# Kernel tuning notes

Measured on AMD Instinct MI355X. Metric: run time of the kernel, lower is better.

Reference implementation:

```python
import jax, jax.numpy as jnp
import numpy as np

B, L = 64, 200
NQ = 1024          # n_question == output_dim
NPID = 4096
D = 256            # q_embed_dim
H = 512            # hidden_dim
Q = 1024           # output_dim
L2 = 1e-05


def setup_inputs() -> dict:
    key = jax.random.key(0)
    ks = jax.random.split(key, 20)
    q_data = jax.random.randint(ks[0], (B, L), 1, NQ + 1)          # question ids in [1, NQ]
    ans = jax.random.randint(ks[1], (B, L), 0, 2)
    qa_data = q_data + NQ * ans                                     # encoded (q, answer)
    pid_data = jax.random.randint(ks[2], (B, L), 0, NPID + 1)
    matrix = jax.random.uniform(ks[3], (Q, Q), jnp.float32) * 0.05  # p_c_relations
    u = jax.random.uniform(ks[4], (B, L))
    target = jnp.where(u < 0.1, -1.0, jnp.where(u < 0.55, 0.0, 1.0)).astype(jnp.float32)
    s = 0.05
    q_emb = jax.random.normal(ks[5], (NQ + 1, D), jnp.float32) * s
    qa_emb = jax.random.normal(ks[6], (2, D), jnp.float32) * s
    q_emb_diff = jax.random.normal(ks[7], (NQ + 1, D), jnp.float32) * s
    qa_emb_diff = jax.random.normal(ks[8], (2 * NQ + 1, D), jnp.float32) * s
    diff_parm = jax.random.normal(ks[9], (NPID + 1, 1), jnp.float32) * s
    gs = 1.0 / np.sqrt(H).astype(np.float32)
    w_ih = jax.random.uniform(ks[10], (3 * H, 2 * D), jnp.float32, -gs, gs)
    w_hh = jax.random.uniform(ks[11], (3 * H, H), jnp.float32, -gs, gs)
    b_ih = jax.random.uniform(ks[12], (3 * H,), jnp.float32, -gs, gs)
    b_hh = jax.random.uniform(ks[13], (3 * H,), jnp.float32, -gs, gs)
    fc_w = jax.random.normal(ks[14], (Q, H), jnp.float32) * 0.02
    fc_b = jnp.zeros((Q,), jnp.float32)
    return dict(q_data=q_data, qa_data=qa_data, pid_data=pid_data, matrix=matrix,
                target=target, q_emb=q_emb, qa_emb=qa_emb, q_emb_diff=q_emb_diff,
                qa_emb_diff=qa_emb_diff, diff_parm=diff_parm, w_ih=w_ih, w_hh=w_hh,
                b_ih=b_ih, b_hh=b_hh, fc_w=fc_w, fc_b=fc_b)


def _gru(x, w_ih, w_hh, b_ih, b_hh):
    # PyTorch GRU, single layer, batch_first. x: [B, L, In]
    xg = jnp.einsum('bli,gi->blg', x, w_ih) + b_ih          # [B, L, 3H]
    def step(h, xg_t):
        hg = h @ w_hh.T + b_hh
        xr, xz, xn = jnp.split(xg_t, 3, axis=-1)
        hr, hz, hn = jnp.split(hg, 3, axis=-1)
        r = jax.nn.sigmoid(xr + hr)
        z = jax.nn.sigmoid(xz + hz)
        n = jnp.tanh(xn + r * hn)
        h_new = (1.0 - z) * n + z * h
        return h_new, h_new
    h0 = jnp.zeros((x.shape[0], w_hh.shape[1]), x.dtype)
    _, hs = jax.lax.scan(step, h0, xg.transpose(1, 0, 2))
    return hs.transpose(1, 0, 2)                             # [B, L, H]


def reference(q_data, qa_data, pid_data, matrix, target, q_emb, qa_emb,
              q_emb_diff, qa_emb_diff, diff_parm, w_ih, w_hh, b_ih, b_hh,
              fc_w, fc_b):
    q_embed = q_emb[q_data]                                  # [B, L, D]
    qa = (qa_data - q_data) // NQ                            # answer in {0,1}
    qa_embed = qa_emb[qa] + q_embed
    pid_embed = diff_parm[pid_data]                          # [B, L, 1]
    q_embed2 = q_embed + pid_embed * q_emb_diff[q_data]
    qa_embed2 = qa_embed + pid_embed * qa_emb_diff[qa]
    c_reg = (pid_embed ** 2).sum() * L2

    x = jnp.concatenate([qa_embed2, q_embed2], axis=-1)      # [B, L, 2D]
    gru_out = _gru(x, w_ih, w_hh, b_ih, b_hh)
    gru_out = jnp.einsum('blh,qh->blq', gru_out, fc_w) + fc_b  # [B, L, Q]

    got = jnp.einsum('blq,kq->blk', gru_out, matrix)         # [B, L, Q]
    master = jnp.where(got >= 0.4, 1.0, got)                 # threshold-to-1 only
    # mastery of the question asked at step t: master[b, t, q-1]
    mvals = jnp.take_along_axis(master, (q_data - 1)[..., None], axis=2)[..., 0]  # [B, L]

    f32 = jnp.float32
    eq = (q_data[:, :, None] == q_data[:, None, :]).astype(f32)   # [B, t, k]
    t_idx = jnp.arange(L)
    tri_strict = (t_idx[:, None] > t_idx[None, :]).astype(f32)    # k < t
    tri_incl = (t_idx[:, None] >= t_idx[None, :]).astype(f32)     # k <= t
    mast = (mvals == 1.0).astype(f32)
    notm = (mvals == 0.0).astype(f32)
    qa1 = (qa == 1).astype(f32)
    qa0 = 1.0 - qa1
    base = eq * tri_strict                                        # [B, L, L]
    mc = jnp.einsum('btk,bk->bt', base, qa1 * mast)   # master_correct
    mi = jnp.einsum('btk,bk->bt', base, qa0 * mast)   # master_incorrect
    nmc = jnp.einsum('btk,bk->bt', base, qa0 * notm)  # no_master_correct
    aa = jnp.einsum('btk,tk->bt', eq, tri_incl)       # answered_all (>= 1)

    arB = jnp.arange(B)
    idx = q_data - 1

    def dina_step(carry, xs):
        guess, slip = carry                            # [B, Q] each
        i_t, m_t, qa_t, mc_t, mi_t, nmc_t, aa_t = xs   # [B] each
        g_upd = jnp.where(m_t == 1.0, mc_t / aa_t,
                          jnp.where(qa_t == 0, 1.0 - nmc_t / aa_t, nmc_t / aa_t))
        upd_slip = (m_t == 1.0) & (qa_t == 0)
        new_g = jnp.where(upd_slip, guess[arB, i_t], g_upd)
        new_s = jnp.where(upd_slip, mi_t / aa_t, slip[arB, i_t])
        guess = guess.at[arB, i_t].set(new_g)
        slip = slip.at[arB, i_t].set(new_s)
        p = (1.0 - new_s) * (m_t * new_g + (1.0 - new_s) * (1.0 - m_t))
        return (guess, slip), p

    init = (jnp.zeros((B, Q), f32), jnp.zeros((B, Q), f32))
    xs = (idx.T, mvals.T, qa.T, mc.T, mi.T, nmc.T, aa.T)
    _, ps = jax.lax.scan(dina_step, init, xs)          # [L, B]
    preds = ps.T.reshape(-1)                           # [B*L]

    labels = target.reshape(-1)
    mask = labels > -0.9
    preds_d = jax.lax.stop_gradient(preds)             # torch detaches via torch.tensor()
    mse_sum = (((preds_d - labels) ** 2) * mask.astype(f32)).sum()
    loss = mse_sum + c_reg
    return (loss, jax.nn.sigmoid(preds_d), mask.sum())
```

## Files before the change

### kernel.cpp

```cpp
#include <hip/hip_runtime.h>
#include <hip/hip_bf16.h>
#include <math.h>

#define BB 64
#define LL 200
#define NQ 1024
#define DD 256
#define HH 512
#define QQ 1024
#define G3 1536
#define BL 12800
#define GBLK 256
#define NWRK 130

#define OFF_ACC   ((size_t)0)
#define OFF_CELLS ((size_t)16)
#define OFF_HA    ((size_t)1056)
#define OFF_AQ    (OFF_HA + 65536)
#define OFF_DQ    (OFF_AQ + 1574400)
#define OFF_BQA   (OFF_DQ + 1574400)
#define OFF_CQA   (OFF_BQA + 3072)
#define OFF_WSUM  (OFF_CQA + 3072)
#define OFF_FCWT  (OFF_WSUM + 393216)
#define OFF_M2    (OFF_FCWT + 524288)
#define OFF_MB    (OFF_M2 + 524288)
#define OFF_XG    (OFF_MB + 1024)
#define OFF_GRUT  (OFF_XG + 19660800)
#define OFF_QINT  (OFF_GRUT + 6553600)
#define OFF_QAINT (OFF_QINT + 12800)
#define OFF_PIDF  (OFF_QAINT + 12800)
#define OFF_MVAL  (OFF_PIDF + 12800)
#define OFF_MC    (OFF_MVAL + 12800)
#define OFF_MI    (OFF_MC + 12800)
#define OFF_NMC   (OFF_MI + 12800)
#define OFF_AA    (OFF_NMC + 12800)
#define OFF_PREDS (OFF_AA + 12800)

typedef float f32x4 __attribute__((ext_vector_type(4)));

__device__ __forceinline__ float wave_sum64(float v) {
    #pragma unroll
    for (int o = 32; o > 0; o >>= 1) v += __shfl_down(v, o, 64);
    return v;
}

__device__ __forceinline__ f32x4 llc_load4(const float* p) {
    f32x4 v;
    asm volatile("global_load_dwordx4 %0, %1, off sc0 sc1" : "=v"(v) : "v"(p));
    return v;
}
__device__ __forceinline__ void llc_wait2(f32x4& a, f32x4& b) {
    asm volatile("s_waitcnt vmcnt(0)" : "+v"(a), "+v"(b));
}
__device__ __forceinline__ void llc_store1(float* p, float v) {
    asm volatile("global_store_dword %0, %1, off sc0 sc1" :: "v"(p), "v"(v) : "memory");
}

__device__ __forceinline__ float quad_sum(float v) {
    float t1 = __int_as_float(__builtin_amdgcn_update_dpp(
        0, __float_as_int(v), 0xB1, 0xF, 0xF, true));
    v += t1;
    float t2 = __int_as_float(__builtin_amdgcn_update_dpp(
        0, __float_as_int(v), 0x4E, 0xF, 0xF, true));
    return v + t2;
}

__global__ __launch_bounds__(256) void prep_meta(
    const int* __restrict__ q_data, const int* __restrict__ qa_data,
    const int* __restrict__ pid_data, const float* __restrict__ diff_parm,
    int* __restrict__ qint, int* __restrict__ qaint, float* __restrict__ pidf,
    float* __restrict__ acc)
{
    int r = blockIdx.x * 256 + threadIdx.x;
    float pp = 0.f;
    if (r < BL) {
        int q = q_data[r];
        qint[r] = q;
        qaint[r] = (qa_data[r] - q) / NQ;
        float pid = diff_parm[pid_data[r]];
        pidf[r] = pid;
        pp = pid * pid;
    }
    pp = wave_sum64(pp);
    __shared__ float sm[4];
    int lane = threadIdx.x & 63, w = threadIdx.x >> 6;
    if (lane == 0) sm[w] = pp;
    __syncthreads();
    if (threadIdx.x == 0) atomicAdd(&acc[0], sm[0] + sm[1] + sm[2] + sm[3]);
}

__global__ __launch_bounds__(256) void wsum_kernel(const float* __restrict__ w_ih,
                                                   float* __restrict__ wsum)
{
    int g = blockIdx.x, d = threadIdx.x;
    wsum[(size_t)g * DD + d] = w_ih[(size_t)g * 2 * DD + d] + w_ih[(size_t)g * 2 * DD + DD + d];
}

__global__ __launch_bounds__(256) void gemm_nt_dual(
    const float* __restrict__ A0, const float* __restrict__ A1, int lda,
    const float* __restrict__ B0, const float* __restrict__ B1, int ldb0, int ldb1,
    float* __restrict__ C0, float* __restrict__ C1, int ldc,
    int M, int N, int K,
    const float* __restrict__ bias0, const float* __restrict__ bias1)
{
    const int z = blockIdx.z;
    const float* A = z ? A1 : A0;
    const float* B = z ? B1 : B0;
    float* C = z ? C1 : C0;
    const int ldb = z ? ldb1 : ldb0;
    const float* bias = z ? bias1 : bias0;

    __shared__ float As[16][65];
    __shared__ float Bs[16][65];
    const int bm = blockIdx.y * 64, bn = blockIdx.x * 64;
    const int tid = threadIdx.x;
    const int tx = tid & 15, ty = tid >> 4;
    const int mm = tid >> 4, kk = tid & 15;
    float acc[4][4] = {};
    float ar[4], br[4];
    #pragma unroll
    for (int i = 0; i < 4; ++i) {
        int m = bm + mm + 16 * i;
        ar[i] = (m < M) ? A[(size_t)m * lda + kk] : 0.f;
        int n = bn + mm + 16 * i;
        br[i] = (n < N) ? B[(size_t)n * ldb + kk] : 0.f;
    }
    for (int k0 = 0; k0 < K; k0 += 16) {
        #pragma unroll
        for (int i = 0; i < 4; ++i) { As[kk][mm + 16 * i] = ar[i]; Bs[kk][mm + 16 * i] = br[i]; }
        __syncthreads();
        int kn = k0 + 16;
        if (kn < K) {
            #pragma unroll
            for (int i = 0; i < 4; ++i) {
                int m = bm + mm + 16 * i;
                ar[i] = (m < M) ? A[(size_t)m * lda + kn + kk] : 0.f;
                int n = bn + mm + 16 * i;
                br[i] = (n < N) ? B[(size_t)n * ldb + kn + kk] : 0.f;
            }
        }
        #pragma unroll
        for (int kq = 0; kq < 16; ++kq) {
            float a[4], b[4];
            #pragma unroll
            for (int i = 0; i < 4; ++i) a[i] = As[kq][ty * 4 + i];
            #pragma unroll
            for (int j = 0; j < 4; ++j) b[j] = Bs[kq][tx * 4 + j];
            #pragma unroll
            for (int i = 0; i < 4; ++i)
                #pragma unroll
                for (int j = 0; j < 4; ++j) acc[i][j] += a[i] * b[j];
        }
        __syncthreads();
    }
    #pragma unroll
    for (int i = 0; i < 4; ++i) {
        int m = bm + ty * 4 + i;
        if (m >= M) continue;
        #pragma unroll
        for (int j = 0; j < 4; ++j) {
            int n = bn + tx * 4 + j;
            if (n >= N) continue;
            C[(size_t)m * ldc + n] = acc[i][j] + (bias ? bias[n] : 0.f);
        }
    }
}

__global__ __launch_bounds__(512) void xgt_kernel(
    const float* __restrict__ Aq, const float* __restrict__ Bqa,
    const float* __restrict__ Cqa, const float* __restrict__ Dq,
    const int* __restrict__ qint, const int* __restrict__ qaint,
    const float* __restrict__ pidf, float* __restrict__ xgT)
{
    const int t = blockIdx.x;
    __shared__ float tile[64][129];
    __shared__ int qs[BB];
    __shared__ int qas[BB];
    __shared__ float ps[BB];
    const int tid = threadIdx.x;
    if (tid < BB) {
        qs[tid] = qint[tid * LL + t];
        qas[tid] = qaint[tid * LL + t];
        ps[tid] = pidf[tid * LL + t];
    }
    __syncthreads();
    for (int g0 = 0; g0 < G3; g0 += 128) {
        #pragma unroll
        for (int it = 0; it < 16; ++it) {
            int idx = it * 512 + tid;
            int b = idx >> 7, gg = idx & 127;
            int g = g0 + gg;
            int q = qs[b], qa = qas[b];
            float pid = ps[b];
            tile[b][gg] = Aq[(size_t)q * G3 + g] + Bqa[(size_t)qa * G3 + g]
                        + pid * (Cqa[(size_t)qa * G3 + g] + Dq[(size_t)q * G3 + g]);
        }
        __syncthreads();
        #pragma unroll
        for (int it = 0; it < 16; ++it) {
            int idx = it * 512 + tid;
            int gg = idx >> 6, b = idx & 63;
            xgT[((size_t)t * G3 + g0 + gg) * BB + b] = tile[b][gg];
        }
        __syncthreads();
    }
}

__global__ __launch_bounds__(512) void gru_persist(
    const float* __restrict__ xgT,
    const float* __restrict__ w_hh,
    const float* __restrict__ b_hh,
    float* __restrict__ hA,
    float* __restrict__ gruT2,
    unsigned int* __restrict__ cells,
    const float* __restrict__ matrix,
    const float* __restrict__ fc_w,
    const float* __restrict__ fc_b,
    float* __restrict__ M2,
    float* __restrict__ mb)
{
    __shared__ float hs[8][512];
    __shared__ float part[8][3][16][8];
    __shared__ float As[16][65];
    __shared__ float Bs[16][65];

    const int tid = threadIdx.x;
    const int bid = blockIdx.x;

    if (bid >= GBLK) {
        const int widx = bid - GBLK;
        if (widx >= 128) {
            const int wv2 = tid >> 6, lane2 = tid & 63;
            const int kb = (widx - 128) * 512 + wv2 * 64;
            for (int i = 0; i < 64; ++i) {
                const float* mrow = matrix + (size_t)(kb + i) * QQ;
                float sacc = 0.f;
                #pragma unroll
                for (int j = 0; j < 16; ++j)
                    sacc += mrow[lane2 + 64 * j] * fc_b[lane2 + 64 * j];
                sacc = wave_sum64(sacc);
                if (lane2 == 0) mb[kb + i] = sacc;
            }
            return;
        }
        const int bm = (widx >> 3) * 64, bn = (widx & 7) * 64;
        const int mm = tid >> 4, kk = tid & 15;
        const int nn = tid & 31, k2 = tid >> 5;
        const int tx = tid & 15, ty = tid >> 4;
        float acc[2][4] = {};
        for (int k0 = 0; k0 < QQ; k0 += 16) {
            if (k0) __syncthreads();
            As[kk][mm]      = matrix[(size_t)(bm + mm) * QQ + k0 + kk];
            As[kk][mm + 32] = matrix[(size_t)(bm + mm + 32) * QQ + k0 + kk];
            Bs[k2][nn]      = fc_w[(size_t)(k0 + k2) * HH + bn + nn];
            Bs[k2][nn + 32] = fc_w[(size_t)(k0 + k2) * HH + bn + nn + 32];
            __syncthreads();
            #pragma unroll
            for (int kq = 0; kq < 16; ++kq) {
                float a0 = As[kq][ty * 2], a1 = As[kq][ty * 2 + 1];
                #pragma unroll
                for (int j = 0; j < 4; ++j) {
                    float bv = Bs[kq][tx * 4 + j];
                    acc[0][j] += a0 * bv;
                    acc[1][j] += a1 * bv;
                }
            }
        }
        #pragma unroll
        for (int i = 0; i < 2; ++i)
            #pragma unroll
            for (int j = 0; j < 4; ++j)
                M2[(size_t)(bm + ty * 2 + i) * HH + bn + tx * 4 + j] = acc[i][j];
        return;
    }

    __builtin_amdgcn_s_setprio(1);

    const int bg = bid >> 5;
    const int j0 = (bid & 31) * 16;
    const int wv = tid >> 6;
    const int lane = tid & 63;
    const int g = lane >> 2;
    const int s = lane & 3;

    f32x4 ws4[3][4];
    #pragma unroll
    for (int gate = 0; gate < 3; ++gate)
        #pragma unroll
        for (int q = 0; q < 4; ++q)
            ws4[gate][q] = *(const f32x4*)&w_hh[
                (size_t)(gate * HH + j0 + g) * HH + wv * 64 + q * 16 + s * 4];

    const int eu = tid >> 3;
    const int eb = tid & 7;
    float bhr = 0.f, bhz = 0.f, bhn = 0.f;
    if (tid < 128) {
        bhr = b_hh[j0 + eu];
        bhz = b_hh[HH + j0 + eu];
        bhn = b_hh[2 * HH + j0 + eu];
    }

    const int b0 = lane >> 4;
    const int c0 = (lane & 15) * 4;

    for (int t = 0; t < LL; ++t) {
        float xr = 0.f, xz = 0.f, xn = 0.f;
        if (tid < 128) {
            const float* xb = xgT + (size_t)t * G3 * BB;
            int col = bg * 8 + eb;
            xr = xb[(size_t)(j0 + eu) * BB + col];
            xz = xb[(size_t)(HH + j0 + eu) * BB + col];
            xn = xb[(size_t)(2 * HH + j0 + eu) * BB + col];
        }
        if (t && tid < 64) {
            const unsigned want = (unsigned)t;
            for (;;) {
                unsigned v = want;
                if (lane < 32)
                    v = __hip_atomic_load(&cells[(bg * 32 + lane) * 4],
                                          __ATOMIC_RELAXED, __HIP_MEMORY_SCOPE_AGENT);
                if (__all((int)(v >= want))) break;
                __builtin_amdgcn_s_sleep(2);
            }
        }
        __syncthreads();

        {
            const float* hcur = hA + (size_t)(t & 1) * (HH * BB);
            const float* p0 = hcur + (size_t)(bg * 8 + b0) * HH + wv * 64 + c0;
            f32x4 va = llc_load4(p0);
            f32x4 vb = llc_load4(p0 + 4 * HH);
            llc_wait2(va, vb);
            *(f32x4*)&hs[wv][b0 * 64 + ((c0 + 8 * b0) & 63)] = va;
            *(f32x4*)&hs[wv][(b0 + 4) * 64 + ((c0 + 8 * b0 + 32) & 63)] = vb;
        }

        float acc[3][8];
        #pragma unroll
        for (int gate = 0; gate < 3; ++gate) {
            #pragma unroll
            for (int b = 0; b < 8; ++b) acc[gate][b] = 0.f;
        }
        #pragma unroll
        for (int q = 0; q < 4; ++q) {
            const int cb = q * 16 + s * 4;
            #pragma unroll
            for (int b = 0; b < 8; ++b) {
                f32x4 h4 = *(const f32x4*)&hs[wv][b * 64 + ((cb + 8 * b) & 63)];
                #pragma unroll
                for (int gate = 0; gate < 3; ++gate) {
                    acc[gate][b] += ws4[gate][q].x * h4.x + ws4[gate][q].y * h4.y
                                  + ws4[gate][q].z * h4.z + ws4[gate][q].w * h4.w;
                }
            }
        }

        #pragma unroll
        for (int gate = 0; gate < 3; ++gate)
            #pragma unroll
            for (int b = 0; b < 8; ++b)
                acc[gate][b] = quad_sum(acc[gate][b]);

        if (s < 3) {
            const int rot = (2 * ((g >> 2) + s)) & 7;
            #pragma unroll
            for (int hp = 0; hp < 4; ++hp) {
                const int b = hp * 2;
                float e0 = (s == 0) ? acc[0][b]     : (s == 1) ? acc[1][b]     : acc[2][b];
                float e1 = (s == 0) ? acc[0][b + 1] : (s == 1) ? acc[1][b + 1] : acc[2][b + 1];
                const int bp = (b + rot) & 7;
                *(float2*)&part[wv][s][g][bp] = make_float2(e0, e1);
            }
        }
        __syncthreads();

        if (tid < 128) {
            const int rb = eu >> 2;
            const int bp0 = (eb + 2 * (rb + 0)) & 7;
            const int bp1 = (eb + 2 * (rb + 1)) & 7;
            const int bp2 = (eb + 2 * (rb + 2)) & 7;
            float sg0 = 0.f, sg1 = 0.f, sg2 = 0.f;
            #pragma unroll
            for (int w = 0; w < 8; ++w) {
                sg0 += part[w][0][eu][bp0];
                sg1 += part[w][1][eu][bp1];
                sg2 += part[w][2][eu][bp2];
            }
            const int ku = j0 + eu;
            float hprev = hs[ku >> 6][eb * 64 + (((ku & 63) + 8 * eb) & 63)];
            float rg = 1.f / (1.f + expf(-(xr + sg0 + bhr)));
            float zg = 1.f / (1.f + expf(-(xz + sg1 + bhz)));
            float ng = tanhf(xn + rg * (sg2 + bhn));
            float hn = (1.f - zg) * ng + zg * hprev;
            llc_store1(hA + (size_t)((t + 1) & 1) * (HH * BB)
                          + (size_t)(bg * 8 + eb) * HH + ku, hn);
            gruT2[((size_t)t * BB + bg * 8 + eb) * HH + ku] = hn;
            asm volatile("s_waitcnt vmcnt(0)" ::: "memory");
        }
        __syncthreads();
        if (tid == 0 && t + 1 < LL)
            __hip_atomic_store(&cells[bid * 4], (unsigned)(t + 1),
                               __ATOMIC_RELAXED, __HIP_MEMORY_SCOPE_AGENT);
    }
}

__global__ __launch_bounds__(256) void mval_kernel(
    const float* __restrict__ gruT2,
    const float* __restrict__ M2,
    const float* __restrict__ mb,
    const int* __restrict__ qint,
    float* __restrict__ mval)
{
    int t = blockIdx.x;
    int wave = threadIdx.x >> 6, l = threadIdx.x & 63;
    for (int ii = 0; ii < 16; ++ii) {
        int b = wave * 16 + ii;
        int q = qint[b * LL + t] - 1;
        const float4* hp = (const float4*)(gruT2 + ((size_t)t * BB + b) * HH);
        const float4* mp = (const float4*)(M2 + (size_t)q * HH);
        float4 h0 = hp[l], m0 = mp[l];
        float4 h1 = hp[64 + l], m1 = mp[64 + l];
        float acc = h0.x * m0.x + h0.y * m0.y + h0.z * m0.z + h0.w * m0.w
                  + h1.x * m1.x + h1.y * m1.y + h1.z * m1.z + h1.w * m1.w;
        acc = wave_sum64(acc);
        if (l == 0) {
            float sv = acc + mb[q];
            mval[b * LL + t] = (sv >= 0.4f) ? 1.0f : sv;
        }
    }
}

__global__ __launch_bounds__(256) void stats_kernel(
    const int* __restrict__ qint, const int* __restrict__ qaint,
    const float* __restrict__ mval,
    float* __restrict__ mc, float* __restrict__ mi,
    float* __restrict__ nmc, float* __restrict__ aa)
{
    int b = blockIdx.x, tid = threadIdx.x;
    __shared__ int qs[LL];
    __shared__ int qas[LL];
    __shared__ float mv[LL];
    if (tid < LL) {
        qs[tid] = qint[b * LL + tid];
        qas[tid] = qaint[b * LL + tid];
        mv[tid] = mval[b * LL + tid];
    }
    __syncthreads();
    int t = tid;
    if (t < LL) {
        int qt = qs[t];
        float smc = 0.f, smi = 0.f, snmc = 0.f, saa = 0.f;
        for (int k = 0; k <= t; ++k) {
            if (qs[k] == qt) {
                saa += 1.f;
                if (k < t) {
                    float mk = (mv[k] == 1.f) ? 1.f : 0.f;
                    float nk = (mv[k] == 0.f) ? 1.f : 0.f;
                    float a1 = (qas[k] == 1) ? 1.f : 0.f;
                    smc += a1 * mk;
                    smi += (1.f - a1) * mk;
                    snmc += (1.f - a1) * nk;
                }
            }
        }
        mc[b * LL + t] = smc;
        mi[b * LL + t] = smi;
        nmc[b * LL + t] = snmc;
        aa[b * LL + t] = saa;
    }
}

__global__ __launch_bounds__(256) void dina_kernel(
    const int* __restrict__ qint, const int* __restrict__ qaint,
    const float* __restrict__ mval,
    const float* __restrict__ mc, const float* __restrict__ mi,
    const float* __restrict__ nmc, const float* __restrict__ aa,
    float* __restrict__ preds)
{
    int b = blockIdx.x, tid = threadIdx.x;
    __shared__ float guess[QQ], slip[QQ];
    __shared__ float s_m[LL], s_mc[LL], s_mi[LL], s_nmc[LL], s_aa[LL];
    __shared__ int s_i[LL], s_qa[LL];
    for (int i = tid; i < QQ; i += 256) { guess[i] = 0.f; slip[i] = 0.f; }
    if (tid < LL) {
        s_m[tid] = mval[b * LL + tid];
        s_mc[tid] = mc[b * LL + tid];
        s_mi[tid] = mi[b * LL + tid];
        s_nmc[tid] = nmc[b * LL + tid];
        s_aa[tid] = aa[b * LL + tid];
        s_i[tid] = qint[b * LL + tid] - 1;
        s_qa[tid] = qaint[b * LL + tid];
    }
    __syncthreads();
    if (tid == 0) {
        for (int t = 0; t < LL; ++t) {
            int i = s_i[t];
            float m = s_m[t];
            int qa = s_qa[t];
            float aat = s_aa[t];
            float g_upd = (m == 1.f) ? s_mc[t] / aat
                          : ((qa == 0) ? 1.f - s_nmc[t] / aat : s_nmc[t] / aat);
            bool us = (m == 1.f) && (qa == 0);
            float ng = us ? guess[i] : g_upd;
            float ns = us ? s_mi[t] / aat : slip[i];
            guess[i] = ng;
            slip[i] = ns;
            preds[b * LL + t] = (1.f - ns) * (m * ng + (1.f - ns) * (1.f - m));
        }
    }
}

__global__ __launch_bounds__(256) void loss_kernel(
    const float* __restrict__ preds, const float* __restrict__ target,
    float* __restrict__ out, float* __restrict__ acc)
{
    int r = blockIdx.x * 256 + threadIdx.x;
    float lm = 0.f, lc = 0.f;
    if (r < BL) {
        float p = preds[r], lab = target[r];
        float msk = (lab > -0.9f) ? 1.f : 0.f;
        float d = p - lab;
        lm = d * d * msk;
        lc = msk;
        out[1 + r] = 1.f / (1.f + expf(-p));
    }
    lm = wave_sum64(lm);
    lc = wave_sum64(lc);
    __shared__ float sm[4], sc[4];
    int lane = threadIdx.x & 63, w = threadIdx.x >> 6;
    if (lane == 0) { sm[w] = lm; sc[w] = lc; }
    __syncthreads();
    if (threadIdx.x == 0) {
        atomicAdd(&acc[1], sm[0] + sm[1] + sm[2] + sm[3]);
        atomicAdd(&acc[2], sc[0] + sc[1] + sc[2] + sc[3]);
    }
}

__global__ void final_kernel(const float* __restrict__ acc, float* __restrict__ out)
{
    out[0] = acc[1] + acc[0] * 1e-5f;
    out[1 + BL] = acc[2];
}

extern "C" void kernel_launch(void* const* d_in, const int* in_sizes, int n_in,
                              void* d_out, int out_size, void* d_ws, size_t ws_size,
                              hipStream_t stream) {
    const int* q_data = (const int*)d_in[0];
    const int* qa_data = (const int*)d_in[1];
    const int* pid_data = (const int*)d_in[2];
    const float* matrix = (const float*)d_in[3];
    const float* target = (const float*)d_in[4];
    const float* q_emb = (const float*)d_in[5];
    const float* qa_emb = (const float*)d_in[6];
    const float* q_emb_diff = (const float*)d_in[7];
    const float* qa_emb_diff = (const float*)d_in[8];
    const float* diff_parm = (const float*)d_in[9];
    const float* w_ih = (const float*)d_in[10];
    const float* w_hh = (const float*)d_in[11];
    const float* b_ih = (const float*)d_in[12];
    const float* b_hh = (const float*)d_in[13];
    const float* fc_w = (const float*)d_in[14];
    const float* fc_b = (const float*)d_in[15];
    float* out = (float*)d_out;
    float* W = (float*)d_ws;

    float* acc = W + OFF_ACC;
    unsigned int* cells = (unsigned int*)(W + OFF_CELLS);
    float* hA = W + OFF_HA;
    float* Aq = W + OFF_AQ;
    float* Dq = W + OFF_DQ;
    float* Bqa = W + OFF_BQA;
    float* Cqa = W + OFF_CQA;
    float* wsum = W + OFF_WSUM;
    float* M2 = W + OFF_M2;
    float* mb = W + OFF_MB;
    float* xgT = W + OFF_XG;
    float* gruT2 = W + OFF_GRUT;
    int* qint = (int*)(W + OFF_QINT);
    int* qaint = (int*)(W + OFF_QAINT);
    float* pidf = W + OFF_PIDF;
    float* mval = W + OFF_MVAL;
    float* mc = W + OFF_MC;
    float* mi = W + OFF_MI;
    float* nmc = W + OFF_NMC;
    float* aa = W + OFF_AA;
    float* preds = W + OFF_PREDS;

    hipMemsetAsync(W, 0, (OFF_HA + 2 * HH * BB) * sizeof(float), stream);

    prep_meta<<<50, 256, 0, stream>>>(q_data, qa_data, pid_data, diff_parm,
                                      qint, qaint, pidf, acc);
    wsum_kernel<<<G3, 256, 0, stream>>>(w_ih, wsum);

    gemm_nt_dual<<<dim3(24, 1, 2), 256, 0, stream>>>(
        qa_emb, qa_emb_diff, DD, w_ih, w_ih, 2 * DD, 2 * DD,
        Bqa, Cqa, G3, 2, G3, DD, b_ih, nullptr);
    gemm_nt_dual<<<dim3(24, 17, 2), 256, 0, stream>>>(
        q_emb, q_emb_diff, DD, wsum, w_ih + DD, DD, 2 * DD,
        Aq, Dq, G3, NQ + 1, G3, DD, nullptr, nullptr);

    xgt_kernel<<<LL, 512, 0, stream>>>(Aq, Bqa, Cqa, Dq, qint, qaint, pidf, xgT);

    gru_persist<<<GBLK + NWRK, 512, 0, stream>>>(xgT, w_hh, b_hh, hA, gruT2, cells,
                                                 matrix, fc_w, fc_b, M2, mb);

    mval_kernel<<<LL, 256, 0, stream>>>(gruT2, M2, mb, qint, mval);
    stats_kernel<<<BB, 256, 0, stream>>>(qint, qaint, mval, mc, mi, nmc, aa);
    dina_kernel<<<BB, 256, 0, stream>>>(qint, qaint, mval, mc, mi, nmc, aa, preds);
    loss_kernel<<<50, 256, 0, stream>>>(preds, target, out, acc);
    final_kernel<<<1, 1, 0, stream>>>(acc, out);
}
```

Before: 1.184 ms.

## Interleave M2/mb side GEMM into idle GRU waves across timesteps

Removes the extra worker blocks that computed M2 = matrix·fc_w and mb = matrix·fc_b alongside the persistent GRU. That work is now spread across the recurrent loop: waves 2-7 of each GRU block compute an 8x64 M2 tile, one k-slice of 8 per timestep for the first 128 steps, and the remaining slots do mb rows at staggered steps. The aim is to use idle wave time during the serial recurrence and drop the extra blocks and the setprio hack. The risk is that the added global loads per step lengthen the GRU critical path, since the wave barrier sync now waits on those waves.

New measurement: 1.405 ms. 18.6% more time.

```diff
diff --git a/kernel.cpp b/kernel.cpp
--- a/kernel.cpp
+++ b/kernel.cpp
@@ -11,7 +11,6 @@
 #define G3 1536
 #define BL 12800
 #define GBLK 256
-#define NWRK 130
 
 #define OFF_ACC   ((size_t)0)
 #define OFF_CELLS ((size_t)16)
@@ -221,61 +220,9 @@
 {
     __shared__ float hs[8][512];
     __shared__ float part[8][3][16][8];
-    __shared__ float As[16][65];
-    __shared__ float Bs[16][65];
 
     const int tid = threadIdx.x;
     const int bid = blockIdx.x;
-
-    if (bid >= GBLK) {
-        const int widx = bid - GBLK;
-        if (widx >= 128) {
-            const int wv2 = tid >> 6, lane2 = tid & 63;
-            const int kb = (widx - 128) * 512 + wv2 * 64;
-            for (int i = 0; i < 64; ++i) {
-                const float* mrow = matrix + (size_t)(kb + i) * QQ;
-                float sacc = 0.f;
-                #pragma unroll
-                for (int j = 0; j < 16; ++j)
-                    sacc += mrow[lane2 + 64 * j] * fc_b[lane2 + 64 * j];
-                sacc = wave_sum64(sacc);
-                if (lane2 == 0) mb[kb + i] = sacc;
-            }
-            return;
-        }
-        const int bm = (widx >> 3) * 64, bn = (widx & 7) * 64;
-        const int mm = tid >> 4, kk = tid & 15;
-        const int nn = tid & 31, k2 = tid >> 5;
-        const int tx = tid & 15, ty = tid >> 4;
-        float acc[2][4] = {};
-        for (int k0 = 0; k0 < QQ; k0 += 16) {
-            if (k0) __syncthreads();
-            As[kk][mm]      = matrix[(size_t)(bm + mm) * QQ + k0 + kk];
-            As[kk][mm + 32] = matrix[(size_t)(bm + mm + 32) * QQ + k0 + kk];
-            Bs[k2][nn]      = fc_w[(size_t)(k0 + k2) * HH + bn + nn];
-            Bs[k2][nn + 32] = fc_w[(size_t)(k0 + k2) * HH + bn + nn + 32];
-            __syncthreads();
-            #pragma unroll
-            for (int kq = 0; kq < 16; ++kq) {
-                float a0 = As[kq][ty * 2], a1 = As[kq][ty * 2 + 1];
-                #pragma unroll
-                for (int j = 0; j < 4; ++j) {
-                    float bv = Bs[kq][tx * 4 + j];
-                    acc[0][j] += a0 * bv;
-                    acc[1][j] += a1 * bv;
-                }
-            }
-        }
-        #pragma unroll
-        for (int i = 0; i < 2; ++i)
-            #pragma unroll
-            for (int j = 0; j < 4; ++j)
-                M2[(size_t)(bm + ty * 2 + i) * HH + bn + tx * 4 + j] = acc[i][j];
-        return;
-    }
-
-    __builtin_amdgcn_s_setprio(1);
-
     const int bg = bid >> 5;
     const int j0 = (bid & 31) * 16;
     const int wv = tid >> 6;
@@ -303,7 +250,49 @@
     const int b0 = lane >> 4;
     const int c0 = (lane & 15) * 4;
 
+    const int slot = bid * 6 + (wv - 2);
+    const bool do_m2 = (wv >= 2) && (slot < 1024);
+    const int r0 = (slot >> 3) << 3;
+    const int n0 = (slot & 7) << 6;
+    const bool do_mb = (wv >= 2) && (slot >= 1024);
+    const int mbrow = (slot - 1024) * 2;
+    const int mbstep = 64 + ((slot - 1024) & 63);
+    float m2acc[8] = {};
+
     for (int t = 0; t < LL; ++t) {
+        if (do_m2) {
+            if (t < 128) {
+                const int k0 = t * 8;
+                float bcol[8];
+                #pragma unroll
+                for (int j = 0; j < 8; ++j)
+                    bcol[j] = fc_w[(size_t)(k0 + j) * HH + n0 + lane];
+                #pragma unroll
+                for (int i = 0; i < 8; ++i) {
+                    f32x4 a0 = *(const f32x4*)&matrix[(size_t)(r0 + i) * QQ + k0];
+                    f32x4 a1 = *(const f32x4*)&matrix[(size_t)(r0 + i) * QQ + k0 + 4];
+                    m2acc[i] += a0.x * bcol[0] + a0.y * bcol[1] + a0.z * bcol[2]
+                              + a0.w * bcol[3] + a1.x * bcol[4] + a1.y * bcol[5]
+                              + a1.z * bcol[6] + a1.w * bcol[7];
+                }
+            } else if (t == 128) {
+                #pragma unroll
+                for (int i = 0; i < 8; ++i)
+                    M2[(size_t)(r0 + i) * HH + n0 + lane] = m2acc[i];
+            }
+        } else if (do_mb && t == mbstep) {
+            #pragma unroll
+            for (int rr = 0; rr < 2; ++rr) {
+                const float* mrow = matrix + (size_t)(mbrow + rr) * QQ;
+                float sacc = 0.f;
+                #pragma unroll
+                for (int j = 0; j < 16; ++j)
+                    sacc += mrow[lane + 64 * j] * fc_b[lane + 64 * j];
+                sacc = wave_sum64(sacc);
+                if (lane == 0) mb[mbrow + rr] = sacc;
+            }
+        }
+
         float xr = 0.f, xz = 0.f, xn = 0.f;
         if (tid < 128) {
             const float* xb = xgT + (size_t)t * G3 * BB;
@@ -601,8 +590,8 @@
 
     xgt_kernel<<<LL, 512, 0, stream>>>(Aq, Bqa, Cqa, Dq, qint, qaint, pidf, xgT);
 
-    gru_persist<<<GBLK + NWRK, 512, 0, stream>>>(xgT, w_hh, b_hh, hA, gruT2, cells,
-                                                 matrix, fc_w, fc_b, M2, mb);
+    gru_persist<<<GBLK, 512, 0, stream>>>(xgT, w_hh, b_hh, hA, gruT2, cells,
+                                          matrix, fc_w, fc_b, M2, mb);
 
     mval_kernel<<<LL, 256, 0, stream>>>(gruT2, M2, mb, qint, mval);
     stats_kernel<<<BB, 256, 0, stream>>>(qint, qaint, mval, mc, mi, nmc, aa);
```

## Fuse input-gate gather into GRU loop and split M2 GEMM out

Applied to the files above, without the earlier changes.

Removes the xgt_kernel that materialized the full [L,3H,B] input-gate tensor. The persistent GRU kernel now gathers Aq/Dq rows by question id each step and combines them with Bqa/Cqa held in shared memory. The M2/mb precompute moves from extra worker blocks of the persistent kernel into its own launch ahead of the GRU, and the embedding GEMM tile grows to 128 rows. This saves roughly 80MB of writes and reads, but puts scattered gathers inside the serial recurrence and makes M2 run before the GRU rather than alongside it.

New measurement: 1.151 ms. 2.8% less time.

```diff
diff --git a/kernel.cpp b/kernel.cpp
--- a/kernel.cpp
+++ b/kernel.cpp
@@ -11,7 +11,6 @@
 #define G3 1536
 #define BL 12800
 #define GBLK 256
-#define NWRK 130
 
 #define OFF_ACC   ((size_t)0)
 #define OFF_CELLS ((size_t)16)
@@ -110,52 +109,60 @@
     const int ldb = z ? ldb1 : ldb0;
     const float* bias = z ? bias1 : bias0;
 
-    __shared__ float As[16][65];
+    __shared__ float As[16][129];
     __shared__ float Bs[16][65];
-    const int bm = blockIdx.y * 64, bn = blockIdx.x * 64;
+    const int bm = blockIdx.y * 128, bn = blockIdx.x * 64;
     const int tid = threadIdx.x;
     const int tx = tid & 15, ty = tid >> 4;
     const int mm = tid >> 4, kk = tid & 15;
-    float acc[4][4] = {};
-    float ar[4], br[4];
+    float acc[8][4] = {};
+    float ar[8], br[4];
+    #pragma unroll
+    for (int i = 0; i < 8; ++i) {
+        int m = bm + mm + 16 * i;
+        ar[i] = (m < M) ? A[(size_t)m * lda + kk] : 0.f;
+    }
     #pragma unroll
     for (int i = 0; i < 4; ++i) {
-        int m = bm + mm + 16 * i;
-        ar[i] = (m < M) ? A[(size_t)m * lda + kk] : 0.f;
         int n = bn + mm + 16 * i;
         br[i] = (n < N) ? B[(size_t)n * ldb + kk] : 0.f;
     }
     for (int k0 = 0; k0 < K; k0 += 16) {
         #pragma unroll
-        for (int i = 0; i < 4; ++i) { As[kk][mm + 16 * i] = ar[i]; Bs[kk][mm + 16 * i] = br[i]; }
+        for (int i = 0; i < 8; ++i) As[kk][mm + 16 * i] = ar[i];
+        #pragma unroll
+        for (int i = 0; i < 4; ++i) Bs[kk][mm + 16 * i] = br[i];
         __syncthreads();
         int kn = k0 + 16;
         if (kn < K) {
             #pragma unroll
-            for (int i = 0; i < 4; ++i) {
+            for (int i = 0; i < 8; ++i) {
                 int m = bm + mm + 16 * i;
                 ar[i] = (m < M) ? A[(size_t)m * lda + kn + kk] : 0.f;
+            }
+            #pragma unroll
+            for (int i = 0; i < 4; ++i) {
                 int n = bn + mm + 16 * i;
                 br[i] = (n < N) ? B[(size_t)n * ldb + kn + kk] : 0.f;
             }
         }
         #pragma unroll
         for (int kq = 0; kq < 16; ++kq) {
-            float a[4], b[4];
-            #pragma unroll
-            for (int i = 0; i < 4; ++i) a[i] = As[kq][ty * 4 + i];
+            float a[8], b[4];
+            #pragma unroll
+            for (int i = 0; i < 8; ++i) a[i] = As[kq][ty * 8 + i];
             #pragma unroll
             for (int j = 0; j < 4; ++j) b[j] = Bs[kq][tx * 4 + j];
             #pragma unroll
-            for (int i = 0; i < 4; ++i)
+            for (int i = 0; i < 8; ++i)
                 #pragma unroll
                 for (int j = 0; j < 4; ++j) acc[i][j] += a[i] * b[j];
         }
         __syncthreads();
     }
     #pragma unroll
-    for (int i = 0; i < 4; ++i) {
-        int m = bm + ty * 4 + i;
+    for (int i = 0; i < 8; ++i) {
+        int m = bm + ty * 8 + i;
         if (m >= M) continue;
         #pragma unroll
         for (int j = 0; j < 4; ++j) {
@@ -166,122 +173,95 @@
     }
 }
 
-__global__ __launch_bounds__(512) void xgt_kernel(
-    const float* __restrict__ Aq, const float* __restrict__ Bqa,
-    const float* __restrict__ Cqa, const float* __restrict__ Dq,
-    const int* __restrict__ qint, const int* __restrict__ qaint,
-    const float* __restrict__ pidf, float* __restrict__ xgT)
-{
-    const int t = blockIdx.x;
-    __shared__ float tile[64][129];
-    __shared__ int qs[BB];
-    __shared__ int qas[BB];
-    __shared__ float ps[BB];
-    const int tid = threadIdx.x;
-    if (tid < BB) {
-        qs[tid] = qint[tid * LL + t];
-        qas[tid] = qaint[tid * LL + t];
-        ps[tid] = pidf[tid * LL + t];
-    }
-    __syncthreads();
-    for (int g0 = 0; g0 < G3; g0 += 128) {
-        #pragma unroll
-        for (int it = 0; it < 16; ++it) {
-            int idx = it * 512 + tid;
-            int b = idx >> 7, gg = idx & 127;
-            int g = g0 + gg;
-            int q = qs[b], qa = qas[b];
-            float pid = ps[b];
-            tile[b][gg] = Aq[(size_t)q * G3 + g] + Bqa[(size_t)qa * G3 + g]
-                        + pid * (Cqa[(size_t)qa * G3 + g] + Dq[(size_t)q * G3 + g]);
-        }
-        __syncthreads();
-        #pragma unroll
-        for (int it = 0; it < 16; ++it) {
-            int idx = it * 512 + tid;
-            int gg = idx >> 6, b = idx & 63;
-            xgT[((size_t)t * G3 + g0 + gg) * BB + b] = tile[b][gg];
-        }
-        __syncthreads();
-    }
-}
-
-__global__ __launch_bounds__(512) void gru_persist(
-    const float* __restrict__ xgT,
-    const float* __restrict__ w_hh,
-    const float* __restrict__ b_hh,
-    float* __restrict__ hA,
-    float* __restrict__ gruT2,
-    unsigned int* __restrict__ cells,
+__global__ __launch_bounds__(512) void m2mb_kernel(
     const float* __restrict__ matrix,
     const float* __restrict__ fc_w,
     const float* __restrict__ fc_b,
     float* __restrict__ M2,
     float* __restrict__ mb)
 {
+    __shared__ float As[16][65];
+    __shared__ float Bs[16][65];
+    const int tid = threadIdx.x;
+    const int widx = blockIdx.x;
+    if (widx >= 128) {
+        const int wv2 = tid >> 6, lane2 = tid & 63;
+        const int kb = (widx - 128) * 512 + wv2 * 64;
+        for (int i = 0; i < 64; ++i) {
+            const float* mrow = matrix + (size_t)(kb + i) * QQ;
+            float sacc = 0.f;
+            #pragma unroll
+            for (int j = 0; j < 16; ++j)
+                sacc += mrow[lane2 + 64 * j] * fc_b[lane2 + 64 * j];
+            sacc = wave_sum64(sacc);
+            if (lane2 == 0) mb[kb + i] = sacc;
+        }
+        return;
+    }
+    const int bm = (widx >> 3) * 64, bn = (widx & 7) * 64;
+    const int mm = tid >> 4, kk = tid & 15;
+    const int nn = tid & 31, k2 = tid >> 5;
+    const int tx = tid & 15, ty = tid >> 4;
+    float acc[2][4] = {};
+    for (int k0 = 0; k0 < QQ; k0 += 16) {
+        if (k0) __syncthreads();
+        As[kk][mm]      = matrix[(size_t)(bm + mm) * QQ + k0 + kk];
+        As[kk][mm + 32] = matrix[(size_t)(bm + mm + 32) * QQ + k0 + kk];
+        Bs[k2][nn]      = fc_w[(size_t)(k0 + k2) * HH + bn + nn];
+        Bs[k2][nn + 32] = fc_w[(size_t)(k0 + k2) * HH + bn + nn + 32];
+        __syncthreads();
+        #pragma unroll
+        for (int kq = 0; kq < 16; ++kq) {
+            float a0 = As[kq][ty * 2], a1 = As[kq][ty * 2 + 1];
+            #pragma unroll
+            for (int j = 0; j < 4; ++j) {
+                float bv = Bs[kq][tx * 4 + j];
+                acc[0][j] += a0 * bv;
+                acc[1][j] += a1 * bv;
+            }
+        }
+    }
+    #pragma unroll
+    for (int i = 0; i < 2; ++i)
+        #pragma unroll
+        for (int j = 0; j < 4; ++j)
+            M2[(size_t)(bm + ty * 2 + i) * HH + bn + tx * 4 + j] = acc[i][j];
+}
+
+__global__ __launch_bounds__(512) void gru_persist(
+    const float* __restrict__ Aq,
+    const float* __restrict__ Dq,
+    const float* __restrict__ Bqa,
+    const float* __restrict__ Cqa,
+    const int* __restrict__ qint,
+    const int* __restrict__ qaint,
+    const float* __restrict__ pidf,
+    const float* __restrict__ w_hh,
+    const float* __restrict__ b_hh,
+    float* __restrict__ hA,
+    float* __restrict__ gruT2,
+    unsigned int* __restrict__ cells)
+{
     __shared__ float hs[8][512];
     __shared__ float part[8][3][16][8];
-    __shared__ float As[16][65];
-    __shared__ float Bs[16][65];
+    __shared__ float bqs[2][3][16];
+    __shared__ float cqs[2][3][16];
 
     const int tid = threadIdx.x;
     const int bid = blockIdx.x;
-
-    if (bid >= GBLK) {
-        const int widx = bid - GBLK;
-        if (widx >= 128) {
-            const int wv2 = tid >> 6, lane2 = tid & 63;
-            const int kb = (widx - 128) * 512 + wv2 * 64;
-            for (int i = 0; i < 64; ++i) {
-                const float* mrow = matrix + (size_t)(kb + i) * QQ;
-                float sacc = 0.f;
-                #pragma unroll
-                for (int j = 0; j < 16; ++j)
-                    sacc += mrow[lane2 + 64 * j] * fc_b[lane2 + 64 * j];
-                sacc = wave_sum64(sacc);
-                if (lane2 == 0) mb[kb + i] = sacc;
-            }
-            return;
-        }
-        const int bm = (widx >> 3) * 64, bn = (widx & 7) * 64;
-        const int mm = tid >> 4, kk = tid & 15;
-        const int nn = tid & 31, k2 = tid >> 5;
-        const int tx = tid & 15, ty = tid >> 4;
-        float acc[2][4] = {};
-        for (int k0 = 0; k0 < QQ; k0 += 16) {
-            if (k0) __syncthreads();
-            As[kk][mm]      = matrix[(size_t)(bm + mm) * QQ + k0 + kk];
-            As[kk][mm + 32] = matrix[(size_t)(bm + mm + 32) * QQ + k0 + kk];
-            Bs[k2][nn]      = fc_w[(size_t)(k0 + k2) * HH + bn + nn];
-            Bs[k2][nn + 32] = fc_w[(size_t)(k0 + k2) * HH + bn + nn + 32];
-            __syncthreads();
-            #pragma unroll
-            for (int kq = 0; kq < 16; ++kq) {
-                float a0 = As[kq][ty * 2], a1 = As[kq][ty * 2 + 1];
-                #pragma unroll
-                for (int j = 0; j < 4; ++j) {
-                    float bv = Bs[kq][tx * 4 + j];
-                    acc[0][j] += a0 * bv;
-                    acc[1][j] += a1 * bv;
-                }
-            }
-        }
-        #pragma unroll
-        for (int i = 0; i < 2; ++i)
-            #pragma unroll
-            for (int j = 0; j < 4; ++j)
-                M2[(size_t)(bm + ty * 2 + i) * HH + bn + tx * 4 + j] = acc[i][j];
-        return;
-    }
-
-    __builtin_amdgcn_s_setprio(1);
-
     const int bg = bid >> 5;
     const int j0 = (bid & 31) * 16;
     const int wv = tid >> 6;
     const int lane = tid & 63;
     const int g = lane >> 2;
     const int s = lane & 3;
+
+    if (tid < 96) {
+        const int qa = tid / 48, rem = tid - qa * 48;
+        const int gate = rem >> 4, u = rem & 15;
+        bqs[qa][gate][u] = Bqa[(size_t)qa * G3 + gate * HH + j0 + u];
+        cqs[qa][gate][u] = Cqa[(size_t)qa * G3 + gate * HH + j0 + u];
+    }
 
     f32x4 ws4[3][4];
     #pragma unroll
@@ -303,14 +283,22 @@
     const int b0 = lane >> 4;
     const int c0 = (lane & 15) * 4;
 
+    __syncthreads();
+
     for (int t = 0; t < LL; ++t) {
         float xr = 0.f, xz = 0.f, xn = 0.f;
         if (tid < 128) {
-            const float* xb = xgT + (size_t)t * G3 * BB;
-            int col = bg * 8 + eb;
-            xr = xb[(size_t)(j0 + eu) * BB + col];
-            xz = xb[(size_t)(HH + j0 + eu) * BB + col];
-            xn = xb[(size_t)(2 * HH + j0 + eu) * BB + col];
+            const int col = bg * 8 + eb;
+            const int q = qint[col * LL + t];
+            const int qa = qaint[col * LL + t];
+            const float pid = pidf[col * LL + t];
+            const float* aq = Aq + (size_t)q * G3 + j0 + eu;
+            const float* dq = Dq + (size_t)q * G3 + j0 + eu;
+            float ar_ = aq[0], az_ = aq[HH], an_ = aq[2 * HH];
+            float dr_ = dq[0], dz_ = dq[HH], dn_ = dq[2 * HH];
+            xr = ar_ + bqs[qa][0][eu] + pid * (cqs[qa][0][eu] + dr_);
+            xz = az_ + bqs[qa][1][eu] + pid * (cqs[qa][1][eu] + dz_);
+            xn = an_ + bqs[qa][2][eu] + pid * (cqs[qa][2][eu] + dn_);
         }
         if (t && tid < 64) {
             const unsigned want = (unsigned)t;
@@ -574,7 +562,6 @@
     float* wsum = W + OFF_WSUM;
     float* M2 = W + OFF_M2;
     float* mb = W + OFF_MB;
-    float* xgT = W + OFF_XG;
     float* gruT2 = W + OFF_GRUT;
     int* qint = (int*)(W + OFF_QINT);
     int* qaint = (int*)(W + OFF_QAINT);
@@ -595,14 +582,14 @@
     gemm_nt_dual<<<dim3(24, 1, 2), 256, 0, stream>>>(
         qa_emb, qa_emb_diff, DD, w_ih, w_ih, 2 * DD, 2 * DD,
         Bqa, Cqa, G3, 2, G3, DD, b_ih, nullptr);
-    gemm_nt_dual<<<dim3(24, 17, 2), 256, 0, stream>>>(
+    gemm_nt_dual<<<dim3(24, 9, 2), 256, 0, stream>>>(
         q_emb, q_emb_diff, DD, wsum, w_ih + DD, DD, 2 * DD,
         Aq, Dq, G3, NQ + 1, G3, DD, nullptr, nullptr);
 
-    xgt_kernel<<<LL, 512, 0, stream>>>(Aq, Bqa, Cqa, Dq, qint, qaint, pidf, xgT);
-
-    gru_persist<<<GBLK + NWRK, 512, 0, stream>>>(xgT, w_hh, b_hh, hA, gruT2, cells,
-                                                 matrix, fc_w, fc_b, M2, mb);
+    m2mb_kernel<<<130, 512, 0, stream>>>(matrix, fc_w, fc_b, M2, mb);
+
+    gru_persist<<<GBLK, 512, 0, stream>>>(Aq, Dq, Bqa, Cqa, qint, qaint, pidf,
+                                          w_hh, b_hh, hA, gruT2, cells);
 
     mval_kernel<<<LL, 256, 0, stream>>>(gruT2, M2, mb, qint, mval);
     stats_kernel<<<BB, 256, 0, stream>>>(qint, qaint, mval, mc, mi, nmc, aa);
```
